# Optimization experiments

Measured on AMD Instinct MI355X. Metric: run time of the kernel, lower is better.

The kernel has to match this reference:

```python
import jax, jax.numpy as jnp
import numpy as np

N_NODES = 100000
N_EDGES = 1600000
D_IN = 128
D_OUT = 128


def setup_inputs() -> dict:
    key = jax.random.key(0)
    k1, k2, k3, k4, k5 = jax.random.split(key, 5)
    x = jax.random.normal(k1, (N_NODES, D_IN), dtype=jnp.float32)
    # glorot_init: uniform in [-r, r], r = sqrt(6/(n_in+n_out))
    r = np.sqrt(6.0 / (D_IN + D_OUT))
    weight = jax.random.uniform(k2, (D_IN, D_OUT), dtype=jnp.float32, minval=-r, maxval=r)
    edge_vals = jax.random.uniform(k3, (N_EDGES,), dtype=jnp.float32)
    edge_rows = jax.random.randint(k4, (N_EDGES,), 0, N_NODES, dtype=jnp.int32)
    edge_cols = jax.random.randint(k5, (N_EDGES,), 0, N_NODES, dtype=jnp.int32)
    return {"x": x, "weight": weight, "edge_vals": edge_vals,
            "edge_rows": edge_rows, "edge_cols": edge_cols}


def reference(x, weight, edge_vals, edge_rows, edge_cols):
    # h = x @ W   [N, d_out]
    h = jnp.matmul(x, weight)
    # spmm: out[r] = sum_{edges e with row r} val_e * h[col_e]
    msg = edge_vals[:, None] * h[edge_cols]          # [E, d_out] gather
    agg = jax.ops.segment_sum(msg, edge_rows, num_segments=N_NODES)  # scatter-add
    return jax.nn.relu(agg)
```

## Files before the change

kernel.cpp:

```cpp
#include <hip/hip_runtime.h>
#include <hip/hip_bf16.h>

#define N_NODES 100000
#define N_EDGES 1600000
#define D 128
#define N_TILES 6250
#define NB 512
#define RPB 196
#define BCAP 3584
#define SA_WGS 768
#define SA_EDGES 2084
#define CAP 12

typedef __bf16 bf16x8 __attribute__((ext_vector_type(8)));
typedef float  f32x4  __attribute__((ext_vector_type(4)));
typedef float  f32x2  __attribute__((ext_vector_type(2)));
typedef int    i32x2  __attribute__((ext_vector_type(2)));

__global__ __launch_bounds__(256) void prep_kernel(const float* __restrict__ W,
                                                   __bf16* __restrict__ WT,
                                                   int* __restrict__ bucketCnt) {
    int t = blockIdx.x * 256 + threadIdx.x;
    int k = t >> 7, n = t & 127;
    WT[n * D + k] = (__bf16)W[t];
    if (t < NB) bucketCnt[t] = 0;
}

__global__ __launch_bounds__(256) void gemm_kernel(
        const float* __restrict__ x,
        const __bf16* __restrict__ WT,
        __bf16* __restrict__ h) {
    __shared__ __bf16 lsm[4][16][144];
    const int wave = threadIdx.x >> 6;
    const int lane = threadIdx.x & 63;
    const int tile = blockIdx.x * 4 + wave;
    if (tile >= N_TILES) return;
    const int m = lane & 15, quad = lane >> 4;
    const float* xp = x + (size_t)(tile * 16 + m) * D + quad * 8;

    f32x4 acc[8];
#pragma unroll
    for (int ct = 0; ct < 8; ++ct) acc[ct] = (f32x4)(0.0f);
#pragma unroll
    for (int kk = 0; kk < 4; ++kk) {
        f32x4 a0 = *(const f32x4*)(xp + kk * 32);
        f32x4 a1 = *(const f32x4*)(xp + kk * 32 + 4);
        bf16x8 a;
#pragma unroll
        for (int j = 0; j < 4; ++j) { a[j] = (__bf16)a0[j]; a[j + 4] = (__bf16)a1[j]; }
#pragma unroll
        for (int ct = 0; ct < 8; ++ct) {
            bf16x8 b = *(const bf16x8*)(WT + (size_t)(ct * 16 + m) * D + kk * 32 + quad * 8);
            acc[ct] = __builtin_amdgcn_mfma_f32_16x16x32_bf16(a, b, acc[ct], 0, 0, 0);
        }
    }
#pragma unroll
    for (int ct = 0; ct < 8; ++ct)
#pragma unroll
        for (int r = 0; r < 4; ++r)
            lsm[wave][quad * 4 + r][ct * 16 + m] = (__bf16)acc[ct][r];
#pragma unroll
    for (int i = 0; i < 4; ++i) {
        int rl = i * 4 + quad;
        bf16x8 vv = *(const bf16x8*)&lsm[wave][rl][m * 8];
        *(bf16x8*)(h + (size_t)(tile * 16 + rl) * D + m * 8) = vv;
    }
}

__global__ __launch_bounds__(256) void scatterA_kernel(
        const int* __restrict__ rows, const int* __restrict__ cols,
        const float* __restrict__ vals,
        int* __restrict__ bucketCnt, i32x2* __restrict__ svcA) {
    __shared__ i32x2 buf[NB][CAP];
    __shared__ int   cnt[NB];
    for (int t = threadIdx.x; t < NB; t += 256) cnt[t] = 0;
    __syncthreads();
    const int base = blockIdx.x * SA_EDGES;
    for (int it = 0; it < 9; ++it) {
        int idx = it * 256 + threadIdx.x;
        if (idx < SA_EDGES) {
            int e = base + idx;
            if (e < N_EDGES) {
                int r = rows[e];
                int b = r / RPB;
                int local = r - b * RPB;
                i32x2 pk;
                pk[0] = (local << 17) | cols[e];
                pk[1] = __float_as_int(vals[e]);
                int p = atomicAdd(&cnt[b], 1);
                if (p < CAP) buf[b][p] = pk;
                else {
                    int g = atomicAdd(&bucketCnt[b], 1);
                    if (g < BCAP) svcA[(size_t)b * BCAP + g] = pk;
                }
            }
        }
    }
    __syncthreads();
    for (int t = threadIdx.x; t < NB; t += 256) {
        int n = min(cnt[t], CAP);
        if (n > 0) {
            int g = atomicAdd(&bucketCnt[t], n);
            i32x2* dst = svcA + (size_t)t * BCAP;
            for (int i = 0; i < n; ++i)
                if (g + i < BCAP) dst[g + i] = buf[t][i];
        }
    }
}

__device__ __forceinline__ f32x2 bf2f(unsigned u) {
    f32x2 r;
    r[0] = __int_as_float(u << 16);
    r[1] = __int_as_float(u & 0xffff0000u);
    return r;
}

__global__ __launch_bounds__(1024, 8) void sortsum_kernel(
        const __bf16* __restrict__ h, const int* __restrict__ bucketCnt,
        const i32x2* __restrict__ svcA, float* __restrict__ out) {
    __shared__ i32x2 lbuf[BCAP];
    __shared__ int   lhist[256];
    __shared__ int   send[256];
    __shared__ int   lcur[256];
    const int b   = blockIdx.x;
    const int tid = threadIdx.x;
    const int n   = min(bucketCnt[b], BCAP);
    const i32x2* win = svcA + (size_t)b * BCAP;

    if (tid < 256) lhist[tid] = 0;
    __syncthreads();

    i32x2 rec0, rec1, rec2, rec3;
    const int i0 = tid, i1 = tid + 1024, i2 = tid + 2048, i3 = tid + 3072;
    if (i0 < n) { rec0 = win[i0]; atomicAdd(&lhist[((unsigned)rec0[0]) >> 17], 1); }
    if (i1 < n) { rec1 = win[i1]; atomicAdd(&lhist[((unsigned)rec1[0]) >> 17], 1); }
    if (i2 < n) { rec2 = win[i2]; atomicAdd(&lhist[((unsigned)rec2[0]) >> 17], 1); }
    if (i3 < n) { rec3 = win[i3]; atomicAdd(&lhist[((unsigned)rec3[0]) >> 17], 1); }
    __syncthreads();

    if (tid < 64) {
        int b0 = lhist[tid * 4 + 0], b1 = lhist[tid * 4 + 1];
        int b2 = lhist[tid * 4 + 2], b3 = lhist[tid * 4 + 3];
        int p0 = b0, p1 = p0 + b1, p2 = p1 + b2, p3 = p2 + b3;
        int s = p3;
#pragma unroll
        for (int d = 1; d < 64; d <<= 1) {
            int t2 = __shfl_up(s, d, 64);
            if (tid >= d) s += t2;
        }
        int ex = s - p3;
        send[tid * 4 + 0] = ex + p0;
        send[tid * 4 + 1] = ex + p1;
        send[tid * 4 + 2] = ex + p2;
        send[tid * 4 + 3] = ex + p3;
        lcur[tid * 4 + 0] = ex;
        lcur[tid * 4 + 1] = ex + p0;
        lcur[tid * 4 + 2] = ex + p1;
        lcur[tid * 4 + 3] = ex + p2;
    }
    __syncthreads();

    if (i0 < n) { int rl = ((unsigned)rec0[0]) >> 17; lbuf[atomicAdd(&lcur[rl], 1)] = rec0; }
    if (i1 < n) { int rl = ((unsigned)rec1[0]) >> 17; lbuf[atomicAdd(&lcur[rl], 1)] = rec1; }
    if (i2 < n) { int rl = ((unsigned)rec2[0]) >> 17; lbuf[atomicAdd(&lcur[rl], 1)] = rec2; }
    if (i3 < n) { int rl = ((unsigned)rec3[0]) >> 17; lbuf[atomicAdd(&lcur[rl], 1)] = rec3; }
    __syncthreads();

    const int wave = tid >> 6;
    const int lane = tid & 63;
    const char* hb = (const char*)h;
    const unsigned lo4 = (unsigned)lane * 4u;
    for (int rl = wave; rl < RPB; rl += 16) {
        int gr = b * RPB + rl;
        if (gr >= N_NODES) break;
        int s = rl ? send[rl - 1] : 0;
        int e = send[rl];

        f32x2 acc0 = (f32x2)(0.0f), acc1 = (f32x2)(0.0f);
        f32x2 acc2 = (f32x2)(0.0f), acc3 = (f32x2)(0.0f);
        int i = s;
        for (; i + 7 < e; i += 8) {
            i32x2 r0 = lbuf[i],     r1 = lbuf[i + 1], r2 = lbuf[i + 2], r3 = lbuf[i + 3];
            i32x2 r4 = lbuf[i + 4], r5 = lbuf[i + 5], r6 = lbuf[i + 6], r7 = lbuf[i + 7];
            unsigned o0 = (((unsigned)r0[0] & 0x1FFFFu) << 8) + lo4;
            unsigned o1 = (((unsigned)r1[0] & 0x1FFFFu) << 8) + lo4;
            unsigned o2 = (((unsigned)r2[0] & 0x1FFFFu) << 8) + lo4;
            unsigned o3 = (((unsigned)r3[0] & 0x1FFFFu) << 8) + lo4;
            unsigned o4 = (((unsigned)r4[0] & 0x1FFFFu) << 8) + lo4;
            unsigned o5 = (((unsigned)r5[0] & 0x1FFFFu) << 8) + lo4;
            unsigned o6 = (((unsigned)r6[0] & 0x1FFFFu) << 8) + lo4;
            unsigned o7 = (((unsigned)r7[0] & 0x1FFFFu) << 8) + lo4;
            unsigned u0 = *(const unsigned*)(hb + o0);
            unsigned u1 = *(const unsigned*)(hb + o1);
            unsigned u2 = *(const unsigned*)(hb + o2);
            unsigned u3 = *(const unsigned*)(hb + o3);
            unsigned u4 = *(const unsigned*)(hb + o4);
            unsigned u5 = *(const unsigned*)(hb + o5);
            unsigned u6 = *(const unsigned*)(hb + o6);
            unsigned u7 = *(const unsigned*)(hb + o7);
            acc0 += bf2f(u0) * __int_as_float(r0[1]);
            acc1 += bf2f(u1) * __int_as_float(r1[1]);
            acc2 += bf2f(u2) * __int_as_float(r2[1]);
            acc3 += bf2f(u3) * __int_as_float(r3[1]);
            acc0 += bf2f(u4) * __int_as_float(r4[1]);
            acc1 += bf2f(u5) * __int_as_float(r5[1]);
            acc2 += bf2f(u6) * __int_as_float(r6[1]);
            acc3 += bf2f(u7) * __int_as_float(r7[1]);
        }
        for (; i + 3 < e; i += 4) {
            i32x2 r0 = lbuf[i], r1 = lbuf[i + 1], r2 = lbuf[i + 2], r3 = lbuf[i + 3];
            unsigned o0 = (((unsigned)r0[0] & 0x1FFFFu) << 8) + lo4;
            unsigned o1 = (((unsigned)r1[0] & 0x1FFFFu) << 8) + lo4;
            unsigned o2 = (((unsigned)r2[0] & 0x1FFFFu) << 8) + lo4;
            unsigned o3 = (((unsigned)r3[0] & 0x1FFFFu) << 8) + lo4;
            unsigned u0 = *(const unsigned*)(hb + o0);
            unsigned u1 = *(const unsigned*)(hb + o1);
            unsigned u2 = *(const unsigned*)(hb + o2);
            unsigned u3 = *(const unsigned*)(hb + o3);
            acc0 += bf2f(u0) * __int_as_float(r0[1]);
            acc1 += bf2f(u1) * __int_as_float(r1[1]);
            acc2 += bf2f(u2) * __int_as_float(r2[1]);
            acc3 += bf2f(u3) * __int_as_float(r3[1]);
        }
        for (; i < e; ++i) {
            i32x2 r0 = lbuf[i];
            unsigned o0 = (((unsigned)r0[0] & 0x1FFFFu) << 8) + lo4;
            unsigned u0 = *(const unsigned*)(hb + o0);
            acc0 += bf2f(u0) * __int_as_float(r0[1]);
        }

        f32x2 t01 = acc0 + acc1, t23 = acc2 + acc3;
        f32x2 tt = t01 + t23;
        f32x2 o;
        o[0] = fmaxf(tt[0], 0.0f);
        o[1] = fmaxf(tt[1], 0.0f);
        __builtin_nontemporal_store(o, (f32x2*)(out + (size_t)gr * D + lane * 2));
    }
}

extern "C" void kernel_launch(void* const* d_in, const int* in_sizes, int n_in,
                              void* d_out, int out_size, void* d_ws, size_t ws_size,
                              hipStream_t stream) {
    const float* x    = (const float*)d_in[0];
    const float* w    = (const float*)d_in[1];
    const float* vals = (const float*)d_in[2];
    const int*   rows = (const int*)d_in[3];
    const int*   cols = (const int*)d_in[4];
    float*       out  = (float*)d_out;

    char* p = (char*)d_ws;
    __bf16* h         = (__bf16*)p;  p += (size_t)N_NODES * D * 2;
    __bf16* WT        = (__bf16*)p;  p += (size_t)D * D * 2;
    int*    bucketCnt = (int*)p;     p += 4096;
    i32x2*  svcA      = (i32x2*)p;   p += (size_t)NB * BCAP * 8;

    prep_kernel<<<64, 256, 0, stream>>>(w, WT, bucketCnt);
    gemm_kernel<<<(N_TILES + 3) / 4, 256, 0, stream>>>(x, WT, h);
    scatterA_kernel<<<SA_WGS, 256, 0, stream>>>(rows, cols, vals, bucketCnt, svcA);
    sortsum_kernel<<<NB, 1024, 0, stream>>>(h, bucketCnt, svcA, out);
}
```

Baseline: 237.3 us.

## Fuse GEMM and edge-bucketing scatter into one interleaved kernel launch

Merges the bf16 MFMA GEMM and the edge bucketing pass into one kernel. Every fourth block does scatter work over 3125 edges and the other three compute GEMM tiles, so the compute-bound GEMM and the memory/atomic-bound scatter run at the same time. This also removes a kernel launch boundary. In exchange, every block now reserves the larger scatter shared-memory footprint, which may cut GEMM occupancy, and the scatter now uses 512 blocks instead of 768, so there is less scatter parallelism.

```diff
diff --git a/kernel.cpp b/kernel.cpp
--- a/kernel.cpp
+++ b/kernel.cpp
@@ -8,9 +8,10 @@
 #define NB 512
 #define RPB 196
 #define BCAP 3584
-#define SA_WGS 768
-#define SA_EDGES 2084
+#define SA_EDGES 3125
 #define CAP 12
+#define GEMM_BLKS 1563
+#define FUSED_BLKS 2084
 
 typedef __bf16 bf16x8 __attribute__((ext_vector_type(8)));
 typedef float  f32x4  __attribute__((ext_vector_type(4)));
@@ -26,64 +27,32 @@
     if (t < NB) bucketCnt[t] = 0;
 }
 
-__global__ __launch_bounds__(256) void gemm_kernel(
+__global__ __launch_bounds__(256) void fused_kernel(
         const float* __restrict__ x,
         const __bf16* __restrict__ WT,
-        __bf16* __restrict__ h) {
-    __shared__ __bf16 lsm[4][16][144];
-    const int wave = threadIdx.x >> 6;
-    const int lane = threadIdx.x & 63;
-    const int tile = blockIdx.x * 4 + wave;
-    if (tile >= N_TILES) return;
-    const int m = lane & 15, quad = lane >> 4;
-    const float* xp = x + (size_t)(tile * 16 + m) * D + quad * 8;
-
-    f32x4 acc[8];
-#pragma unroll
-    for (int ct = 0; ct < 8; ++ct) acc[ct] = (f32x4)(0.0f);
-#pragma unroll
-    for (int kk = 0; kk < 4; ++kk) {
-        f32x4 a0 = *(const f32x4*)(xp + kk * 32);
-        f32x4 a1 = *(const f32x4*)(xp + kk * 32 + 4);
-        bf16x8 a;
-#pragma unroll
-        for (int j = 0; j < 4; ++j) { a[j] = (__bf16)a0[j]; a[j + 4] = (__bf16)a1[j]; }
-#pragma unroll
-        for (int ct = 0; ct < 8; ++ct) {
-            bf16x8 b = *(const bf16x8*)(WT + (size_t)(ct * 16 + m) * D + kk * 32 + quad * 8);
-            acc[ct] = __builtin_amdgcn_mfma_f32_16x16x32_bf16(a, b, acc[ct], 0, 0, 0);
-        }
-    }
-#pragma unroll
-    for (int ct = 0; ct < 8; ++ct)
-#pragma unroll
-        for (int r = 0; r < 4; ++r)
-            lsm[wave][quad * 4 + r][ct * 16 + m] = (__bf16)acc[ct][r];
-#pragma unroll
-    for (int i = 0; i < 4; ++i) {
-        int rl = i * 4 + quad;
-        bf16x8 vv = *(const bf16x8*)&lsm[wave][rl][m * 8];
-        *(bf16x8*)(h + (size_t)(tile * 16 + rl) * D + m * 8) = vv;
-    }
-}
-
-__global__ __launch_bounds__(256) void scatterA_kernel(
+        __bf16* __restrict__ h,
         const int* __restrict__ rows, const int* __restrict__ cols,
         const float* __restrict__ vals,
         int* __restrict__ bucketCnt, i32x2* __restrict__ svcA) {
-    __shared__ i32x2 buf[NB][CAP];
-    __shared__ int   cnt[NB];
-    for (int t = threadIdx.x; t < NB; t += 256) cnt[t] = 0;
-    __syncthreads();
-    const int base = blockIdx.x * SA_EDGES;
-    for (int it = 0; it < 9; ++it) {
-        int idx = it * 256 + threadIdx.x;
-        if (idx < SA_EDGES) {
-            int e = base + idx;
-            if (e < N_EDGES) {
-                int r = rows[e];
-                int b = r / RPB;
-                int local = r - b * RPB;
+    __shared__ __align__(16) char smem[NB * CAP * 8 + NB * 4];
+    const int bid = blockIdx.x;
+    const int g4 = bid >> 2, r = bid & 3;
+
+    if (r == 3) {
+        const int sb = g4;
+        if (sb >= NB) return;
+        i32x2 (*buf)[CAP] = (i32x2 (*)[CAP])smem;
+        int*  cnt = (int*)(smem + (size_t)NB * CAP * 8);
+        for (int t = threadIdx.x; t < NB; t += 256) cnt[t] = 0;
+        __syncthreads();
+        const int base = sb * SA_EDGES;
+        for (int it = 0; it < 13; ++it) {
+            int idx = it * 256 + threadIdx.x;
+            if (idx < SA_EDGES) {
+                int e = base + idx;
+                int rr = rows[e];
+                int b = rr / RPB;
+                int local = rr - b * RPB;
                 i32x2 pk;
                 pk[0] = (local << 17) | cols[e];
                 pk[1] = __float_as_int(vals[e]);
@@ -95,15 +64,52 @@
                 }
             }
         }
-    }
-    __syncthreads();
-    for (int t = threadIdx.x; t < NB; t += 256) {
-        int n = min(cnt[t], CAP);
-        if (n > 0) {
-            int g = atomicAdd(&bucketCnt[t], n);
-            i32x2* dst = svcA + (size_t)t * BCAP;
-            for (int i = 0; i < n; ++i)
-                if (g + i < BCAP) dst[g + i] = buf[t][i];
+        __syncthreads();
+        for (int t = threadIdx.x; t < NB; t += 256) {
+            int n = min(cnt[t], CAP);
+            if (n > 0) {
+                int g = atomicAdd(&bucketCnt[t], n);
+                i32x2* dst = svcA + (size_t)t * BCAP;
+                for (int i = 0; i < n; ++i)
+                    if (g + i < BCAP) dst[g + i] = buf[t][i];
+            }
+        }
+    } else {
+        const int gid = g4 * 3 + r;
+        __bf16 (*lsm)[16][144] = (__bf16 (*)[16][144])smem;
+        const int wave = threadIdx.x >> 6;
+        const int lane = threadIdx.x & 63;
+        const int tile = gid * 4 + wave;
+        if (tile >= N_TILES) return;
+        const int m = lane & 15, quad = lane >> 4;
+        const float* xp = x + (size_t)(tile * 16 + m) * D + quad * 8;
+
+        f32x4 acc[8];
+#pragma unroll
+        for (int ct = 0; ct < 8; ++ct) acc[ct] = (f32x4)(0.0f);
+#pragma unroll
+        for (int kk = 0; kk < 4; ++kk) {
+            f32x4 a0 = *(const f32x4*)(xp + kk * 32);
+            f32x4 a1 = *(const f32x4*)(xp + kk * 32 + 4);
+            bf16x8 a;
+#pragma unroll
+            for (int j = 0; j < 4; ++j) { a[j] = (__bf16)a0[j]; a[j + 4] = (__bf16)a1[j]; }
+#pragma unroll
+            for (int ct = 0; ct < 8; ++ct) {
+                bf16x8 b = *(const bf16x8*)(WT + (size_t)(ct * 16 + m) * D + kk * 32 + quad * 8);
+                acc[ct] = __builtin_amdgcn_mfma_f32_16x16x32_bf16(a, b, acc[ct], 0, 0, 0);
+            }
+        }
+#pragma unroll
+        for (int ct = 0; ct < 8; ++ct)
+#pragma unroll
+            for (int rr = 0; rr < 4; ++rr)
+                lsm[wave][quad * 4 + rr][ct * 16 + m] = (__bf16)acc[ct][rr];
+#pragma unroll
+        for (int i = 0; i < 4; ++i) {
+            int rl = i * 4 + quad;
+            bf16x8 vv = *(const bf16x8*)&lsm[wave][rl][m * 8];
+            *(bf16x8*)(h + (size_t)(tile * 16 + rl) * D + m * 8) = vv;
         }
     }
 }
@@ -255,7 +261,7 @@
     i32x2*  svcA      = (i32x2*)p;   p += (size_t)NB * BCAP * 8;
 
     prep_kernel<<<64, 256, 0, stream>>>(w, WT, bucketCnt);
-    gemm_kernel<<<(N_TILES + 3) / 4, 256, 0, stream>>>(x, WT, h);
-    scatterA_kernel<<<SA_WGS, 256, 0, stream>>>(rows, cols, vals, bucketCnt, svcA);
+    fused_kernel<<<FUSED_BLKS, 256, 0, stream>>>(x, WT, h, rows, cols, vals,
+                                                 bucketCnt, svcA);
     sortsum_kernel<<<NB, 1024, 0, stream>>>(h, bucketCnt, svcA, out);
 }
```

Result: faster. 228.5 us (-3.7%).

## Replace capped shared-buffer edge binning with per-block counting sort

Applied to the files above, without the earlier changes.

The edge bucketing kernel now uses 256 workgroups of 1024 threads, each handling 6250 edges. Each block builds a local histogram over the 512 buckets, computes an exclusive scan with wave shuffles, and sorts the records into shared memory. It then flushes each bucket with one global atomic and a contiguous copy. This drops the old fixed 12-slot per-bucket buffer and its overflow path, which issued global atomics and scattered writes per edge. In exchange, the per-bucket flush loop is serial per thread and writes about 12 records each, and fewer, larger blocks give less parallelism.

```diff
diff --git a/kernel.cpp b/kernel.cpp
--- a/kernel.cpp
+++ b/kernel.cpp
@@ -8,9 +8,8 @@
 #define NB 512
 #define RPB 196
 #define BCAP 3584
-#define SA_WGS 768
-#define SA_EDGES 2084
-#define CAP 12
+#define SB_BLKS 256
+#define SB_EDGES 6250
 
 typedef __bf16 bf16x8 __attribute__((ext_vector_type(8)));
 typedef float  f32x4  __attribute__((ext_vector_type(4)));
@@ -67,43 +66,75 @@
     }
 }
 
-__global__ __launch_bounds__(256) void scatterA_kernel(
+__global__ __launch_bounds__(1024, 8) void scatterB_kernel(
         const int* __restrict__ rows, const int* __restrict__ cols,
         const float* __restrict__ vals,
         int* __restrict__ bucketCnt, i32x2* __restrict__ svcA) {
-    __shared__ i32x2 buf[NB][CAP];
-    __shared__ int   cnt[NB];
-    for (int t = threadIdx.x; t < NB; t += 256) cnt[t] = 0;
-    __syncthreads();
-    const int base = blockIdx.x * SA_EDGES;
-    for (int it = 0; it < 9; ++it) {
-        int idx = it * 256 + threadIdx.x;
-        if (idx < SA_EDGES) {
-            int e = base + idx;
-            if (e < N_EDGES) {
-                int r = rows[e];
-                int b = r / RPB;
-                int local = r - b * RPB;
-                i32x2 pk;
-                pk[0] = (local << 17) | cols[e];
-                pk[1] = __float_as_int(vals[e]);
-                int p = atomicAdd(&cnt[b], 1);
-                if (p < CAP) buf[b][p] = pk;
-                else {
-                    int g = atomicAdd(&bucketCnt[b], 1);
-                    if (g < BCAP) svcA[(size_t)b * BCAP + g] = pk;
-                }
-            }
-        }
-    }
-    __syncthreads();
-    for (int t = threadIdx.x; t < NB; t += 256) {
-        int n = min(cnt[t], CAP);
+    __shared__ i32x2 lbuf[SB_EDGES];
+    __shared__ int   lhist[NB];
+    __shared__ int   sstart[NB];
+    __shared__ int   lcur[NB];
+    const int tid  = threadIdx.x;
+    const int base = blockIdx.x * SB_EDGES;
+
+    if (tid < NB) lhist[tid] = 0;
+    __syncthreads();
+
+    i32x2 r0, r1, r2, r3, r4, r5, r6;
+    int   b0, b1, b2, b3, b4, b5, b6;
+#define LOADREC(K, RK, BK)                                             \
+    {                                                                  \
+        int e = base + tid + (K) * 1024;                               \
+        int rr = rows[e];                                              \
+        BK = rr / RPB;                                                 \
+        int local = rr - BK * RPB;                                     \
+        RK[0] = (local << 17) | cols[e];                               \
+        RK[1] = __float_as_int(vals[e]);                               \
+        atomicAdd(&lhist[BK], 1);                                      \
+    }
+    LOADREC(0, r0, b0) LOADREC(1, r1, b1) LOADREC(2, r2, b2)
+    LOADREC(3, r3, b3) LOADREC(4, r4, b4) LOADREC(5, r5, b5)
+    if (tid < SB_EDGES - 6 * 1024) { LOADREC(6, r6, b6) }
+#undef LOADREC
+    __syncthreads();
+
+    if (tid < 64) {
+        const int bb = tid * 8;
+        int run = 0;
+#pragma unroll
+        for (int j = 0; j < 8; ++j) run += lhist[bb + j];
+        int s = run;
+#pragma unroll
+        for (int d = 1; d < 64; d <<= 1) {
+            int t2 = __shfl_up(s, d, 64);
+            if (tid >= d) s += t2;
+        }
+        int ex = s - run;
+#pragma unroll
+        for (int j = 0; j < 8; ++j) {
+            sstart[bb + j] = ex;
+            lcur[bb + j]   = ex;
+            ex += lhist[bb + j];
+        }
+    }
+    __syncthreads();
+
+    lbuf[atomicAdd(&lcur[b0], 1)] = r0;
+    lbuf[atomicAdd(&lcur[b1], 1)] = r1;
+    lbuf[atomicAdd(&lcur[b2], 1)] = r2;
+    lbuf[atomicAdd(&lcur[b3], 1)] = r3;
+    lbuf[atomicAdd(&lcur[b4], 1)] = r4;
+    lbuf[atomicAdd(&lcur[b5], 1)] = r5;
+    if (tid < SB_EDGES - 6 * 1024) lbuf[atomicAdd(&lcur[b6], 1)] = r6;
+    __syncthreads();
+
+    if (tid < NB) {
+        int n = lhist[tid];
         if (n > 0) {
-            int g = atomicAdd(&bucketCnt[t], n);
-            i32x2* dst = svcA + (size_t)t * BCAP;
+            int g = atomicAdd(&bucketCnt[tid], n);
+            int s = sstart[tid];
             for (int i = 0; i < n; ++i)
-                if (g + i < BCAP) dst[g + i] = buf[t][i];
+                if (g + i < BCAP) svcA[(size_t)tid * BCAP + g + i] = lbuf[s + i];
         }
     }
 }
@@ -256,6 +287,6 @@
 
     prep_kernel<<<64, 256, 0, stream>>>(w, WT, bucketCnt);
     gemm_kernel<<<(N_TILES + 3) / 4, 256, 0, stream>>>(x, WT, h);
-    scatterA_kernel<<<SA_WGS, 256, 0, stream>>>(rows, cols, vals, bucketCnt, svcA);
+    scatterB_kernel<<<SB_BLKS, 1024, 0, stream>>>(rows, cols, vals, bucketCnt, svcA);
     sortsum_kernel<<<NB, 1024, 0, stream>>>(h, bucketCnt, svcA, out);
 }
```

New measurement: 220.4 us. -7.1%, faster.
